# Kernel optimization log

Measured on AMD Instinct MI355X. Metric: run time of the kernel, lower is better.

Reference implementation:

```python
import jax, jax.numpy as jnp
import numpy as np

# dims: batch B, tokens T, model_dim D, expert hidden H, experts E, top-k K
B, T, D, H, E, K = 4, 2048, 2048, 2048, 8, 2
CAP_FACTOR = 1.0
S = B * T
C = int(np.ceil(K * S / E * CAP_FACTOR))  # per-expert capacity = 2048


def setup_inputs() -> dict:
    key = jax.random.key(0)
    k0, k1, k2, k3 = jax.random.split(key, 4)
    x = jax.random.normal(k0, (B, T, D), dtype=jnp.float32)
    wg = jax.random.normal(k1, (D, E), dtype=jnp.float32) * (D ** -0.5)
    w1 = jax.random.normal(k2, (E, D, H), dtype=jnp.float32) * (D ** -0.5)
    b1 = jnp.zeros((E, H), dtype=jnp.float32)
    w2 = jax.random.normal(k3, (E, H, D), dtype=jnp.float32) * (H ** -0.5)
    b2 = jnp.zeros((E, D), dtype=jnp.float32)
    return {"x": x, "wg": wg, "w1": w1, "b1": b1, "w2": w2, "b2": b2}


def _moe(x, wg, w1, b1, w2, b2):
    xt = x.reshape(S, D)
    # --- top-k gating (deepspeed-style, gates normalized over selected k) ---
    gates = jax.nn.softmax(xt @ wg, axis=-1)            # [S,E]
    vals, idx = jax.lax.top_k(gates, K)                 # [S,K]
    vals = vals / jnp.sum(vals, axis=-1, keepdims=True)
    # --- capacity-aware slot assignment (slot j offset by counts of slots < j) ---
    m = jax.nn.one_hot(idx, E, dtype=jnp.int32).transpose(1, 0, 2)  # [K,S,E]
    within = jnp.cumsum(m, axis=1) - m                  # 0-based rank within expert per slot
    counts = jnp.sum(m, axis=1)                         # [K,E]
    offs = jnp.cumsum(counts, axis=0) - counts          # [K,E] offsets from earlier slots
    loc = jnp.sum((within + offs[:, None, :]) * m, axis=2)  # [K,S]
    eid = idx.T                                         # [K,S]
    valid = loc < C
    loc_c = jnp.minimum(loc, C - 1)
    # --- dispatch: scatter raw tokens into [E,C,D] expert buffers ---
    contrib = jnp.where(valid[..., None], xt[None, :, :], 0.0)   # [K,S,D]
    disp = jnp.zeros((E, C, D), x.dtype).at[eid, loc_c].add(contrib)
    # --- grouped expert FFN: relu(x @ W1 + b1) @ W2 + b2 ---
    h = jax.nn.relu(jnp.einsum('ecd,edh->ech', disp, w1) + b1[:, None, :])
    ye = jnp.einsum('ech,ehd->ecd', h, w2) + b2[:, None, :]
    # --- combine: gather expert outputs, weight by normalized gates ---
    gathered = ye[eid, loc_c]                           # [K,S,D]
    w = (vals.T * valid).astype(x.dtype)                # [K,S]
    out = jnp.einsum('ks,ksd->sd', w, gathered)
    return out.reshape(B, T, D)


def reference(x, wg, w1, b1, w2, b2):
    y = _moe(x, wg, w1, b1, w2, b2)                     # [B,T,D]
    return jax.nn.log_softmax(jnp.sum(y, axis=2), axis=1)  # [B,T]
```

## Files before the change

### kernel.cpp

```cpp
#include <hip/hip_runtime.h>
#include <math.h>

#define S_TOK 8192
#define DDIM 2048
#define HDIM 2048
#define NE 8
#define CAP 2048
#define NBATCH 4
#define TT 2048

typedef _Float16 f16;
typedef _Float16 f16x4 __attribute__((ext_vector_type(4)));
typedef _Float16 f16x8 __attribute__((ext_vector_type(8)));
typedef float f32x4 __attribute__((ext_vector_type(4)));

typedef __attribute__((address_space(1))) const void* gas_ptr;
typedef __attribute__((address_space(3))) void* las_ptr;

__global__ __launch_bounds__(256) void gating_kernel(const float* __restrict__ x,
                                                     const float* __restrict__ wg,
                                                     int* __restrict__ eid,
                                                     float* __restrict__ wts,
                                                     int* __restrict__ slot_token,
                                                     float* __restrict__ zacc) {
  if (blockIdx.x < 64) {
    int i = blockIdx.x * 256 + threadIdx.x;
    slot_token[i] = 0;
    zacc[i] = 0.f;
  }
  int wid = threadIdx.x >> 6;
  int lane = threadIdx.x & 63;
  int s = blockIdx.x * 4 + wid;
  const float* xr = x + (size_t)s * DDIM;
  double acc[8];
#pragma unroll
  for (int e = 0; e < 8; ++e) acc[e] = 0.0;
  for (int d0 = 0; d0 < DDIM; d0 += 64) {
    float xs = xr[d0 + lane];
    const float4* wp = (const float4*)(wg + (size_t)(d0 + lane) * 8);
    float4 g0 = wp[0];
    float4 g1 = wp[1];
    double xd = (double)xs;
    acc[0] += xd * (double)g0.x; acc[1] += xd * (double)g0.y;
    acc[2] += xd * (double)g0.z; acc[3] += xd * (double)g0.w;
    acc[4] += xd * (double)g1.x; acc[5] += xd * (double)g1.y;
    acc[6] += xd * (double)g1.z; acc[7] += xd * (double)g1.w;
  }
#pragma unroll
  for (int e = 0; e < 8; ++e) {
    double v = acc[e];
    for (int off = 32; off > 0; off >>= 1) v += __shfl_down(v, off, 64);
    acc[e] = v;
  }
  if (lane == 0) {
    int e0 = 0; double l0 = acc[0];
    for (int e = 1; e < 8; ++e) if (acc[e] > l0) { l0 = acc[e]; e0 = e; }
    int e1 = -1; double l1 = -1e300;
    for (int e = 0; e < 8; ++e) if (e != e0 && acc[e] > l1) { l1 = acc[e]; e1 = e; }
    double pe = exp(l1 - l0);
    double inv = 1.0 / (1.0 + pe);
    eid[2 * s] = e0; eid[2 * s + 1] = e1;
    wts[2 * s] = (float)inv; wts[2 * s + 1] = (float)(pe * inv);
  }
}

__global__ __launch_bounds__(256) void scan_kernel(const int* __restrict__ eid,
                                                   int* __restrict__ locb,
                                                   int* __restrict__ slot_token) {
  __shared__ int seg[4][2][8];
  __shared__ int base[4][2][8];
  int tid = threadIdx.x, wid = tid >> 6, lane = tid & 63;
  unsigned long long lower = (lane == 0) ? 0ull : ((~0ull) >> (64 - lane));
  const int2* eid2 = (const int2*)eid;
  int c0 = 0, c1 = 0;
  for (int r = 0; r < 32; ++r) {
    int2 ee = eid2[wid * 2048 + r * 64 + lane];
#pragma unroll
    for (int e = 0; e < 8; ++e) {
      unsigned long long b0 = __ballot(ee.x == e);
      unsigned long long b1 = __ballot(ee.y == e);
      if (lane == e) { c0 += __popcll(b0); c1 += __popcll(b1); }
    }
  }
  if (lane < 8) { seg[wid][0][lane] = c0; seg[wid][1][lane] = c1; }
  __syncthreads();
  if (lane < 8) {
    int e = lane;
    int tot0 = seg[0][0][e] + seg[1][0][e] + seg[2][0][e] + seg[3][0][e];
    int b0 = 0, b1 = tot0;
    for (int w = 0; w < wid; ++w) { b0 += seg[w][0][e]; b1 += seg[w][1][e]; }
    base[wid][0][e] = b0; base[wid][1][e] = b1;
  }
  for (int r = 0; r < 32; ++r) {
    int2 ee = eid2[wid * 2048 + r * 64 + lane];
    int rank0 = 0, rank1 = 0, add0 = 0, add1 = 0;
#pragma unroll
    for (int e = 0; e < 8; ++e) {
      unsigned long long b0 = __ballot(ee.x == e);
      unsigned long long b1 = __ballot(ee.y == e);
      if (ee.x == e) rank0 = __popcll(b0 & lower);
      if (ee.y == e) rank1 = __popcll(b1 & lower);
      if (lane == e) { add0 = __popcll(b0); add1 = __popcll(b1); }
    }
    int loc0 = base[wid][0][ee.x] + rank0;
    int loc1 = base[wid][1][ee.y] + rank1;
    int s = wid * 2048 + r * 64 + lane;
    int2 lo; lo.x = loc0; lo.y = loc1;
    *(int2*)&locb[2 * s] = lo;
    if (loc0 < CAP) slot_token[ee.x * CAP + loc0] = s;
    if (loc1 < CAP) slot_token[ee.y * CAP + loc1] = s;
    if (lane < 8) {
      atomicAdd(&base[wid][0][lane], add0);
      atomicAdd(&base[wid][1][lane], add1);
    }
  }
}

#define W1T_BLOCKS 8192
#define W2S_BLOCKS 4096
#define ABUILD_BASE (W1T_BLOCKS + W2S_BLOCKS + 1)
__global__ __launch_bounds__(256) void prep_kernel(const float* __restrict__ w1,
                                                   const float* __restrict__ w2,
                                                   const float* __restrict__ b2,
                                                   const float* __restrict__ x,
                                                   const int* __restrict__ slot_token,
                                                   f16* __restrict__ W1T,
                                                   float* __restrict__ w2s,
                                                   float* __restrict__ b2s,
                                                   f16* __restrict__ A16) {
  __shared__ float tile[64 * 65];
  int bid = blockIdx.x, tid = threadIdx.x;
  if (bid >= ABUILD_BASE) {
    int slot = bid - ABUILD_BASE;
    int s = slot_token[slot];
    const float4* x4 = (const float4*)x + (size_t)s * 512;
    f16x4* outp = (f16x4*)(A16 + (size_t)slot * DDIM);
#pragma unroll
    for (int i = 0; i < 2; ++i) {
      int v = i * 256 + tid;
      float4 xv = x4[v];
      f16x4 h;
      h[0] = (f16)xv.x; h[1] = (f16)xv.y; h[2] = (f16)xv.z; h[3] = (f16)xv.w;
      outp[v] = h;
    }
    return;
  }
  if (bid < W1T_BLOCKS) {
    int e = bid >> 10, rem = bid & 1023;
    int d0 = (rem >> 5) << 6;
    int h0 = (rem & 31) << 6;
    const float* w1e = w1 + (size_t)e * DDIM * HDIM;
#pragma unroll
    for (int i = 0; i < 4; ++i) {
      int linear = i * 256 + tid;
      int r = linear >> 4, c4 = linear & 15;
      float4 v = *(const float4*)(w1e + (size_t)(d0 + r) * HDIM + h0 + c4 * 4);
      float* t = &tile[r * 65 + c4 * 4];
      t[0] = v.x; t[1] = v.y; t[2] = v.z; t[3] = v.w;
    }
    __syncthreads();
    f16* W1Te = W1T + (size_t)e * HDIM * DDIM;
#pragma unroll
    for (int i = 0; i < 2; ++i) {
      int linear = i * 256 + tid;
      int hr = linear >> 3, l8 = linear & 7;
      f16x8 o;
#pragma unroll
      for (int j = 0; j < 8; ++j) o[j] = (f16)tile[(l8 * 8 + j) * 65 + hr];
      *(f16x8*)(W1Te + (size_t)(h0 + hr) * DDIM + d0 + l8 * 8) = o;
    }
    return;
  }
  if (bid < W1T_BLOCKS + W2S_BLOCKS) {
    int wid = tid >> 6, lane = tid & 63;
    int row = (bid - W1T_BLOCKS) * 4 + wid;
    const float4* w24 = (const float4*)w2;
    float acc = 0.f;
    for (int j = 0; j < 8; ++j) {
      float4 v = w24[(size_t)row * 512 + j * 64 + lane];
      acc += v.x + v.y + v.z + v.w;
    }
    for (int off = 32; off > 0; off >>= 1) acc += __shfl_down(acc, off, 64);
    if (lane == 0) w2s[row] = acc;
    return;
  }
  {
    int e = tid >> 5, l32 = tid & 31;
    float acc = 0.f;
    for (int j = 0; j < 64; ++j) acc += b2[e * 2048 + j * 32 + l32];
    for (int off = 16; off > 0; off >>= 1) acc += __shfl_down(acc, off, 32);
    if (l32 == 0) b2s[e] = acc;
  }
}


template <int MB, int NB>
__device__ __forceinline__ void quad_mfma(f32x4 (&acc)[8][4], const f16x8 (&av)[4][2],
                                          const f16x8 (&bv)[2][2]) {
#pragma unroll
  for (int mf = 0; mf < 4; ++mf)
#pragma unroll
    for (int nf = 0; nf < 2; ++nf) {
      f32x4 c = acc[MB + mf][NB + nf];
      c = __builtin_amdgcn_mfma_f32_16x16x32_f16(av[mf][0], bv[nf][0], c, 0, 0, 0);
      c = __builtin_amdgcn_mfma_f32_16x16x32_f16(av[mf][1], bv[nf][1], c, 0, 0, 0);
      acc[MB + mf][NB + nf] = c;
    }
}

__device__ __forceinline__ void lda4(f16x8 (&av)[4][2], const f16* p0, const f16* p1, int mh) {
#pragma unroll
  for (int mf = 0; mf < 4; ++mf) {
    av[mf][0] = *(const f16x8*)(p0 + (mh * 4 + mf) * 1024);
    av[mf][1] = *(const f16x8*)(p1 + (mh * 4 + mf) * 1024);
  }
}
__device__ __forceinline__ void ldb2(f16x8 (&bv)[2][2], const f16* p0, const f16* p1, int nh) {
#pragma unroll
  for (int nf = 0; nf < 2; ++nf) {
    bv[nf][0] = *(const f16x8*)(p0 + (nh * 2 + nf) * 1024);
    bv[nf][1] = *(const f16x8*)(p1 + (nh * 2 + nf) * 1024);
  }
}

__device__ __forceinline__ void stage_half(const f16* tile_rows, f16* lds_region,
                                           int T, int h, int wl8, int wu8, int cs) {
#pragma unroll
  for (int i = 0; i < 2; ++i) {
    const f16* g = tile_rows + (size_t)(h * 128 + i * 64 + wl8) * DDIM + T * 64 + cs * 8;
    f16* d = lds_region + (h * 128 + i * 64 + wu8) * 64;
    __builtin_amdgcn_global_load_lds((gas_ptr)g, (las_ptr)d, 16, 0, 0);
  }
}

__device__ __forceinline__ void bar() {
  asm volatile("" ::: "memory");
  __builtin_amdgcn_s_barrier();
  asm volatile("" ::: "memory");
}
__device__ __forceinline__ void mfma_open() {
  bar();
  asm volatile("s_waitcnt lgkmcnt(0)" ::: "memory");
  __builtin_amdgcn_sched_barrier(0);
  __builtin_amdgcn_s_setprio(1);
}
__device__ __forceinline__ void mfma_close() {
  __builtin_amdgcn_s_setprio(0);
  bar();
}
__device__ __forceinline__ void mfma_close_w4() {
  __builtin_amdgcn_s_setprio(0);
  asm volatile("s_waitcnt vmcnt(4)" ::: "memory");
  bar();
}
__device__ __forceinline__ void mfma_close_w0() {
  __builtin_amdgcn_s_setprio(0);
  asm volatile("s_waitcnt vmcnt(0)" ::: "memory");
  bar();
}

__global__ __launch_bounds__(512, 2) void gemm_kernel(const f16* __restrict__ A16,
                                                      const f16* __restrict__ W1T,
                                                      const float* __restrict__ b1,
                                                      const float* __restrict__ w2s,
                                                      float* __restrict__ zacc) {
  __shared__ __align__(16) f16 lds[4 * 256 * 64];
  const int tid = threadIdx.x;
  const int wid = tid >> 6, lane = tid & 63;
  const int wm = wid >> 2, wn = wid & 3;
  const int quad = lane >> 4, l15 = lane & 15;
  const int l3 = lane >> 3, c7 = lane & 7;
  const int cs = c7 ^ l3;
  const int wl8 = wid * 8 + l3, wu8 = wid * 8;

  int bid = blockIdx.x;
  int e = bid & 7;
  int idx = bid >> 3;
  int cT = idx >> 3, hT = idx & 7;
  int c0 = cT * 256, h0 = hT * 256;

  const f16* Abase = A16 + ((size_t)e * CAP + c0) * DDIM;
  const f16* Bbase = W1T + ((size_t)e * HDIM + h0) * DDIM;

  f16* bufA0 = &lds[0];
  f16* bufB0 = &lds[16384];
  f16* bufA1 = &lds[2 * 16384];
  f16* bufB1 = &lds[3 * 16384];

  const int so0 = (quad ^ c7) * 8;
  const int so1 = ((quad + 4) ^ c7) * 8;
  const f16* a0k0 = bufA0 + (wm * 128 + l15) * 64 + so0;
  const f16* a0k1 = bufA0 + (wm * 128 + l15) * 64 + so1;
  const f16* a1k0 = a0k0 + 2 * 16384;
  const f16* a1k1 = a0k1 + 2 * 16384;
  const f16* b0k0 = bufB0 + (wn * 64 + l15) * 64 + so0;
  const f16* b0k1 = bufB0 + (wn * 64 + l15) * 64 + so1;
  const f16* b1k0 = b0k0 + 2 * 16384;
  const f16* b1k1 = b0k1 + 2 * 16384;

  f32x4 acc[8][4];
#pragma unroll
  for (int i = 0; i < 8; ++i)
#pragma unroll
    for (int jj = 0; jj < 4; ++jj) acc[i][jj] = (f32x4){0.f, 0.f, 0.f, 0.f};
  f16x8 fa[4][2], fb0[2][2], fb1[2][2];

  stage_half(Abase, bufA0, 0, 0, wl8, wu8, cs);
  stage_half(Abase, bufA0, 0, 1, wl8, wu8, cs);
  stage_half(Bbase, bufB0, 0, 0, wl8, wu8, cs);
  stage_half(Bbase, bufB0, 0, 1, wl8, wu8, cs);
  stage_half(Bbase, bufB1, 1, 0, wl8, wu8, cs);
  stage_half(Bbase, bufB1, 1, 1, wl8, wu8, cs);
  asm volatile("s_waitcnt vmcnt(4)" ::: "memory");
  bar();

#pragma unroll 1
  for (int it = 0; it < 15; ++it) {
    const int Ta = 2 * it + 1, Tb = 2 * it + 2, Tc = 2 * it + 3;
    lda4(fa, a0k0, a0k1, 0);
    ldb2(fb0, b0k0, b0k1, 0);
    stage_half(Abase, bufA1, Ta, 0, wl8, wu8, cs);
    mfma_open(); quad_mfma<0, 0>(acc, fa, fb0); mfma_close();

    ldb2(fb1, b0k0, b0k1, 1);
    stage_half(Abase, bufA1, Ta, 1, wl8, wu8, cs);
    mfma_open(); quad_mfma<0, 2>(acc, fa, fb1); mfma_close();

    lda4(fa, a0k0, a0k1, 1);
    stage_half(Bbase, bufB0, Tb, 0, wl8, wu8, cs);
    mfma_open(); quad_mfma<4, 2>(acc, fa, fb1); mfma_close();

    stage_half(Bbase, bufB0, Tb, 1, wl8, wu8, cs);
    mfma_open(); quad_mfma<4, 0>(acc, fa, fb0); mfma_close_w4();

    lda4(fa, a1k0, a1k1, 0);
    ldb2(fb0, b1k0, b1k1, 0);
    stage_half(Abase, bufA0, Tb, 0, wl8, wu8, cs);
    mfma_open(); quad_mfma<0, 0>(acc, fa, fb0); mfma_close();

    ldb2(fb1, b1k0, b1k1, 1);
    stage_half(Abase, bufA0, Tb, 1, wl8, wu8, cs);
    mfma_open(); quad_mfma<0, 2>(acc, fa, fb1); mfma_close();

    lda4(fa, a1k0, a1k1, 1);
    stage_half(Bbase, bufB1, Tc, 0, wl8, wu8, cs);
    mfma_open(); quad_mfma<4, 2>(acc, fa, fb1); mfma_close();

    stage_half(Bbase, bufB1, Tc, 1, wl8, wu8, cs);
    mfma_open(); quad_mfma<4, 0>(acc, fa, fb0); mfma_close_w4();
  }
  {
    lda4(fa, a0k0, a0k1, 0);
    ldb2(fb0, b0k0, b0k1, 0);
    stage_half(Abase, bufA1, 31, 0, wl8, wu8, cs);
    mfma_open(); quad_mfma<0, 0>(acc, fa, fb0); mfma_close();

    ldb2(fb1, b0k0, b0k1, 1);
    stage_half(Abase, bufA1, 31, 1, wl8, wu8, cs);
    mfma_open(); quad_mfma<0, 2>(acc, fa, fb1); mfma_close();

    lda4(fa, a0k0, a0k1, 1);
    mfma_open(); quad_mfma<4, 2>(acc, fa, fb1); mfma_close();

    mfma_open(); quad_mfma<4, 0>(acc, fa, fb0); mfma_close_w0();

    lda4(fa, a1k0, a1k1, 0);
    ldb2(fb0, b1k0, b1k1, 0);
    mfma_open(); quad_mfma<0, 0>(acc, fa, fb0); mfma_close();

    ldb2(fb1, b1k0, b1k1, 1);
    mfma_open(); quad_mfma<0, 2>(acc, fa, fb1); mfma_close();

    lda4(fa, a1k0, a1k1, 1);
    mfma_open(); quad_mfma<4, 2>(acc, fa, fb1); mfma_close();

    mfma_open(); quad_mfma<4, 0>(acc, fa, fb0);
    __builtin_amdgcn_s_setprio(0);
  }

  float b1v[4], wsv[4];
#pragma unroll
  for (int nf = 0; nf < 4; ++nf) {
    int h = h0 + wn * 64 + nf * 16 + l15;
    b1v[nf] = b1[e * HDIM + h];
    wsv[nf] = w2s[e * HDIM + h];
  }
#pragma unroll
  for (int mf = 0; mf < 8; ++mf) {
    float pr[4];
#pragma unroll
    for (int rr = 0; rr < 4; ++rr) {
      float t = 0.f;
#pragma unroll
      for (int nf = 0; nf < 4; ++nf) {
        float v = acc[mf][nf][rr] + b1v[nf];
        t += (v > 0.f ? v : 0.f) * wsv[nf];
      }
      pr[rr] = t;
    }
#pragma unroll
    for (int rr = 0; rr < 4; ++rr)
#pragma unroll
      for (int off = 1; off < 16; off <<= 1) pr[rr] += __shfl_xor(pr[rr], off, 64);
    if (l15 == 0) {
      int m = c0 + wm * 128 + mf * 16 + quad * 4;
#pragma unroll
      for (int rr = 0; rr < 4; ++rr) atomicAdd(&zacc[e * CAP + m + rr], pr[rr]);
    }
  }
}

__global__ __launch_bounds__(256) void tail_kernel(const int* __restrict__ eid,
                                                   const int* __restrict__ locb,
                                                   const float* __restrict__ wts,
                                                   const float* __restrict__ zacc,
                                                   const float* __restrict__ b2s,
                                                   float* __restrict__ out) {
  __shared__ float red[4];
  int b = blockIdx.x, tid = threadIdx.x;
  int wid = tid >> 6, lane = tid & 63;
  float v[8];
  float mx = -1e30f;
#pragma unroll
  for (int i = 0; i < 8; ++i) {
    int s = b * TT + i * 256 + tid;
    float zz = 0.f;
#pragma unroll
    for (int k = 0; k < 2; ++k) {
      int e = eid[2 * s + k], loc = locb[2 * s + k];
      if (loc < CAP) zz += wts[2 * s + k] * (zacc[e * CAP + loc] + b2s[e]);
    }
    v[i] = zz;
    mx = fmaxf(mx, zz);
  }
  for (int off = 32; off > 0; off >>= 1) mx = fmaxf(mx, __shfl_xor(mx, off, 64));
  if (lane == 0) red[wid] = mx;
  __syncthreads();
  mx = fmaxf(fmaxf(red[0], red[1]), fmaxf(red[2], red[3]));
  float sum = 0.f;
#pragma unroll
  for (int i = 0; i < 8; ++i) sum += expf(v[i] - mx);
  for (int off = 32; off > 0; off >>= 1) sum += __shfl_xor(sum, off, 64);
  __syncthreads();
  if (lane == 0) red[wid] = sum;
  __syncthreads();
  sum = red[0] + red[1] + red[2] + red[3];
  float lse = mx + logf(sum);
#pragma unroll
  for (int i = 0; i < 8; ++i) out[b * TT + i * 256 + tid] = v[i] - lse;
}

extern "C" void kernel_launch(void* const* d_in, const int* in_sizes, int n_in,
                              void* d_out, int out_size, void* d_ws, size_t ws_size,
                              hipStream_t stream) {
  const float* x  = (const float*)d_in[0];
  const float* wg = (const float*)d_in[1];
  const float* w1 = (const float*)d_in[2];
  const float* b1 = (const float*)d_in[3];
  const float* w2 = (const float*)d_in[4];
  const float* b2 = (const float*)d_in[5];
  float* out = (float*)d_out;

  char* ws = (char*)d_ws;
  size_t off = 0;
  auto alloc = [&](size_t bytes) -> char* {
    char* p = ws + off;
    off += (bytes + 255) & ~(size_t)255;
    return p;
  };
  f16* A16 = (f16*)alloc((size_t)NE * CAP * DDIM * 2);
  f16* W1T = (f16*)alloc((size_t)NE * HDIM * DDIM * 2);
  float* w2s = (float*)alloc((size_t)NE * HDIM * 4);
  float* b2s = (float*)alloc(NE * 4);
  int* eid = (int*)alloc((size_t)S_TOK * 2 * 4);
  float* wts = (float*)alloc((size_t)S_TOK * 2 * 4);
  int* locb = (int*)alloc((size_t)S_TOK * 2 * 4);
  int* slot_token = (int*)alloc((size_t)NE * CAP * 4);
  float* zacc = (float*)alloc((size_t)NE * CAP * 4);
  if (off > ws_size) return;

  gating_kernel<<<S_TOK / 4, 256, 0, stream>>>(x, wg, eid, wts, slot_token, zacc);
  scan_kernel<<<1, 256, 0, stream>>>(eid, locb, slot_token);
  prep_kernel<<<ABUILD_BASE + NE * CAP, 256, 0, stream>>>(w1, w2, b2, x, slot_token,
                                                          W1T, w2s, b2s, A16);
  gemm_kernel<<<NE * 64, 512, 0, stream>>>(A16, W1T, b1, w2s, zacc);
  tail_kernel<<<NBATCH, 256, 0, stream>>>(eid, locb, wts, zacc, b2s, out);
}
```

Baseline: 545.8 us.

## Fuse gating into weight-prep kernel and split A-buffer build into own kernel

Gating now runs inside the weight-preparation launch as extra blocks, so the W1 transpose/convert and w2/b2 reductions overlap with gating instead of waiting behind it. The gather of tokens into the fp16 expert buffer moves to a separate kernel that runs after the scan and uses one wave per slot. The tail kernel goes from 256 to 1024 threads per block to spread its work wider. This changes the launch order and dependencies (the scan now waits on the larger fused kernel) and adds one more kernel launch.

After: 541.4 us. Within noise of the previous version (-0.8%).

```diff
diff --git a/kernel.cpp b/kernel.cpp
--- a/kernel.cpp
+++ b/kernel.cpp
@@ -17,50 +17,113 @@
 typedef __attribute__((address_space(1))) const void* gas_ptr;
 typedef __attribute__((address_space(3))) void* las_ptr;
 
-__global__ __launch_bounds__(256) void gating_kernel(const float* __restrict__ x,
-                                                     const float* __restrict__ wg,
-                                                     int* __restrict__ eid,
-                                                     float* __restrict__ wts,
-                                                     int* __restrict__ slot_token,
-                                                     float* __restrict__ zacc) {
-  if (blockIdx.x < 64) {
-    int i = blockIdx.x * 256 + threadIdx.x;
-    slot_token[i] = 0;
-    zacc[i] = 0.f;
-  }
-  int wid = threadIdx.x >> 6;
-  int lane = threadIdx.x & 63;
-  int s = blockIdx.x * 4 + wid;
-  const float* xr = x + (size_t)s * DDIM;
-  double acc[8];
-#pragma unroll
-  for (int e = 0; e < 8; ++e) acc[e] = 0.0;
-  for (int d0 = 0; d0 < DDIM; d0 += 64) {
-    float xs = xr[d0 + lane];
-    const float4* wp = (const float4*)(wg + (size_t)(d0 + lane) * 8);
-    float4 g0 = wp[0];
-    float4 g1 = wp[1];
-    double xd = (double)xs;
-    acc[0] += xd * (double)g0.x; acc[1] += xd * (double)g0.y;
-    acc[2] += xd * (double)g0.z; acc[3] += xd * (double)g0.w;
-    acc[4] += xd * (double)g1.x; acc[5] += xd * (double)g1.y;
-    acc[6] += xd * (double)g1.z; acc[7] += xd * (double)g1.w;
-  }
-#pragma unroll
-  for (int e = 0; e < 8; ++e) {
-    double v = acc[e];
-    for (int off = 32; off > 0; off >>= 1) v += __shfl_down(v, off, 64);
-    acc[e] = v;
-  }
-  if (lane == 0) {
-    int e0 = 0; double l0 = acc[0];
-    for (int e = 1; e < 8; ++e) if (acc[e] > l0) { l0 = acc[e]; e0 = e; }
-    int e1 = -1; double l1 = -1e300;
-    for (int e = 0; e < 8; ++e) if (e != e0 && acc[e] > l1) { l1 = acc[e]; e1 = e; }
-    double pe = exp(l1 - l0);
-    double inv = 1.0 / (1.0 + pe);
-    eid[2 * s] = e0; eid[2 * s + 1] = e1;
-    wts[2 * s] = (float)inv; wts[2 * s + 1] = (float)(pe * inv);
+#define W1T_BLOCKS 8192
+#define W2S_BLOCKS 4096
+#define GATE_BASE (W1T_BLOCKS + W2S_BLOCKS + 1)
+#define K1_GRID (GATE_BASE + S_TOK / 4)
+
+__global__ __launch_bounds__(256) void prep_kernel(const float* __restrict__ w1,
+                                                   const float* __restrict__ w2,
+                                                   const float* __restrict__ b2,
+                                                   const float* __restrict__ x,
+                                                   const float* __restrict__ wg,
+                                                   int* __restrict__ eid,
+                                                   float* __restrict__ wts,
+                                                   int* __restrict__ slot_token,
+                                                   float* __restrict__ zacc,
+                                                   f16* __restrict__ W1T,
+                                                   float* __restrict__ w2s,
+                                                   float* __restrict__ b2s) {
+  __shared__ float tile[64 * 65];
+  int bid = blockIdx.x, tid = threadIdx.x;
+  if (bid >= GATE_BASE) {
+    int g = bid - GATE_BASE;
+    if (g < 64) {
+      int i = g * 256 + tid;
+      slot_token[i] = 0;
+      zacc[i] = 0.f;
+    }
+    int wid = tid >> 6;
+    int lane = tid & 63;
+    int s = g * 4 + wid;
+    const float* xr = x + (size_t)s * DDIM;
+    double acc[8];
+#pragma unroll
+    for (int e = 0; e < 8; ++e) acc[e] = 0.0;
+    for (int d0 = 0; d0 < DDIM; d0 += 64) {
+      float xs = xr[d0 + lane];
+      const float4* wp = (const float4*)(wg + (size_t)(d0 + lane) * 8);
+      float4 g0 = wp[0];
+      float4 g1 = wp[1];
+      double xd = (double)xs;
+      acc[0] += xd * (double)g0.x; acc[1] += xd * (double)g0.y;
+      acc[2] += xd * (double)g0.z; acc[3] += xd * (double)g0.w;
+      acc[4] += xd * (double)g1.x; acc[5] += xd * (double)g1.y;
+      acc[6] += xd * (double)g1.z; acc[7] += xd * (double)g1.w;
+    }
+#pragma unroll
+    for (int e = 0; e < 8; ++e) {
+      double v = acc[e];
+      for (int off = 32; off > 0; off >>= 1) v += __shfl_down(v, off, 64);
+      acc[e] = v;
+    }
+    if (lane == 0) {
+      int e0 = 0; double l0 = acc[0];
+      for (int e = 1; e < 8; ++e) if (acc[e] > l0) { l0 = acc[e]; e0 = e; }
+      int e1 = -1; double l1 = -1e300;
+      for (int e = 0; e < 8; ++e) if (e != e0 && acc[e] > l1) { l1 = acc[e]; e1 = e; }
+      double pe = exp(l1 - l0);
+      double inv = 1.0 / (1.0 + pe);
+      eid[2 * s] = e0; eid[2 * s + 1] = e1;
+      wts[2 * s] = (float)inv; wts[2 * s + 1] = (float)(pe * inv);
+    }
+    return;
+  }
+  if (bid < W1T_BLOCKS) {
+    int e = bid >> 10, rem = bid & 1023;
+    int d0 = (rem >> 5) << 6;
+    int h0 = (rem & 31) << 6;
+    const float* w1e = w1 + (size_t)e * DDIM * HDIM;
+#pragma unroll
+    for (int i = 0; i < 4; ++i) {
+      int linear = i * 256 + tid;
+      int r = linear >> 4, c4 = linear & 15;
+      float4 v = *(const float4*)(w1e + (size_t)(d0 + r) * HDIM + h0 + c4 * 4);
+      float* t = &tile[r * 65 + c4 * 4];
+      t[0] = v.x; t[1] = v.y; t[2] = v.z; t[3] = v.w;
+    }
+    __syncthreads();
+    f16* W1Te = W1T + (size_t)e * HDIM * DDIM;
+#pragma unroll
+    for (int i = 0; i < 2; ++i) {
+      int linear = i * 256 + tid;
+      int hr = linear >> 3, l8 = linear & 7;
+      f16x8 o;
+#pragma unroll
+      for (int j = 0; j < 8; ++j) o[j] = (f16)tile[(l8 * 8 + j) * 65 + hr];
+      *(f16x8*)(W1Te + (size_t)(h0 + hr) * DDIM + d0 + l8 * 8) = o;
+    }
+    return;
+  }
+  if (bid < W1T_BLOCKS + W2S_BLOCKS) {
+    int wid = tid >> 6, lane = tid & 63;
+    int row = (bid - W1T_BLOCKS) * 4 + wid;
+    const float4* w24 = (const float4*)w2;
+    float acc = 0.f;
+    for (int j = 0; j < 8; ++j) {
+      float4 v = w24[(size_t)row * 512 + j * 64 + lane];
+      acc += v.x + v.y + v.z + v.w;
+    }
+    for (int off = 32; off > 0; off >>= 1) acc += __shfl_down(acc, off, 64);
+    if (lane == 0) w2s[row] = acc;
+    return;
+  }
+  {
+    int e = tid >> 5, l32 = tid & 31;
+    float acc = 0.f;
+    for (int j = 0; j < 64; ++j) acc += b2[e * 2048 + j * 32 + l32];
+    for (int off = 16; off > 0; off >>= 1) acc += __shfl_down(acc, off, 32);
+    if (l32 == 0) b2s[e] = acc;
   }
 }
 
@@ -116,80 +179,20 @@
   }
 }
 
-#define W1T_BLOCKS 8192
-#define W2S_BLOCKS 4096
-#define ABUILD_BASE (W1T_BLOCKS + W2S_BLOCKS + 1)
-__global__ __launch_bounds__(256) void prep_kernel(const float* __restrict__ w1,
-                                                   const float* __restrict__ w2,
-                                                   const float* __restrict__ b2,
-                                                   const float* __restrict__ x,
-                                                   const int* __restrict__ slot_token,
-                                                   f16* __restrict__ W1T,
-                                                   float* __restrict__ w2s,
-                                                   float* __restrict__ b2s,
-                                                   f16* __restrict__ A16) {
-  __shared__ float tile[64 * 65];
-  int bid = blockIdx.x, tid = threadIdx.x;
-  if (bid >= ABUILD_BASE) {
-    int slot = bid - ABUILD_BASE;
-    int s = slot_token[slot];
-    const float4* x4 = (const float4*)x + (size_t)s * 512;
-    f16x4* outp = (f16x4*)(A16 + (size_t)slot * DDIM);
-#pragma unroll
-    for (int i = 0; i < 2; ++i) {
-      int v = i * 256 + tid;
-      float4 xv = x4[v];
-      f16x4 h;
-      h[0] = (f16)xv.x; h[1] = (f16)xv.y; h[2] = (f16)xv.z; h[3] = (f16)xv.w;
-      outp[v] = h;
-    }
-    return;
-  }
-  if (bid < W1T_BLOCKS) {
-    int e = bid >> 10, rem = bid & 1023;
-    int d0 = (rem >> 5) << 6;
-    int h0 = (rem & 31) << 6;
-    const float* w1e = w1 + (size_t)e * DDIM * HDIM;
-#pragma unroll
-    for (int i = 0; i < 4; ++i) {
-      int linear = i * 256 + tid;
-      int r = linear >> 4, c4 = linear & 15;
-      float4 v = *(const float4*)(w1e + (size_t)(d0 + r) * HDIM + h0 + c4 * 4);
-      float* t = &tile[r * 65 + c4 * 4];
-      t[0] = v.x; t[1] = v.y; t[2] = v.z; t[3] = v.w;
-    }
-    __syncthreads();
-    f16* W1Te = W1T + (size_t)e * HDIM * DDIM;
-#pragma unroll
-    for (int i = 0; i < 2; ++i) {
-      int linear = i * 256 + tid;
-      int hr = linear >> 3, l8 = linear & 7;
-      f16x8 o;
-#pragma unroll
-      for (int j = 0; j < 8; ++j) o[j] = (f16)tile[(l8 * 8 + j) * 65 + hr];
-      *(f16x8*)(W1Te + (size_t)(h0 + hr) * DDIM + d0 + l8 * 8) = o;
-    }
-    return;
-  }
-  if (bid < W1T_BLOCKS + W2S_BLOCKS) {
-    int wid = tid >> 6, lane = tid & 63;
-    int row = (bid - W1T_BLOCKS) * 4 + wid;
-    const float4* w24 = (const float4*)w2;
-    float acc = 0.f;
-    for (int j = 0; j < 8; ++j) {
-      float4 v = w24[(size_t)row * 512 + j * 64 + lane];
-      acc += v.x + v.y + v.z + v.w;
-    }
-    for (int off = 32; off > 0; off >>= 1) acc += __shfl_down(acc, off, 64);
-    if (lane == 0) w2s[row] = acc;
-    return;
-  }
-  {
-    int e = tid >> 5, l32 = tid & 31;
-    float acc = 0.f;
-    for (int j = 0; j < 64; ++j) acc += b2[e * 2048 + j * 32 + l32];
-    for (int off = 16; off > 0; off >>= 1) acc += __shfl_down(acc, off, 32);
-    if (l32 == 0) b2s[e] = acc;
+__global__ __launch_bounds__(256) void abuild_kernel(const float* __restrict__ x,
+                                                     const int* __restrict__ slot_token,
+                                                     f16* __restrict__ A16) {
+  int wid = threadIdx.x >> 6, lane = threadIdx.x & 63;
+  int slot = blockIdx.x * 4 + wid;
+  int s = slot_token[slot];
+  const float4* x4 = (const float4*)x + (size_t)s * 512 + lane;
+  f16x4* outp = (f16x4*)(A16 + (size_t)slot * DDIM) + lane;
+#pragma unroll
+  for (int i = 0; i < 8; ++i) {
+    float4 xv = x4[i * 64];
+    f16x4 h;
+    h[0] = (f16)xv.x; h[1] = (f16)xv.y; h[2] = (f16)xv.z; h[3] = (f16)xv.w;
+    outp[i * 64] = h;
   }
 }
 
@@ -410,20 +413,20 @@
   }
 }
 
-__global__ __launch_bounds__(256) void tail_kernel(const int* __restrict__ eid,
-                                                   const int* __restrict__ locb,
-                                                   const float* __restrict__ wts,
-                                                   const float* __restrict__ zacc,
-                                                   const float* __restrict__ b2s,
-                                                   float* __restrict__ out) {
-  __shared__ float red[4];
+__global__ __launch_bounds__(1024) void tail_kernel(const int* __restrict__ eid,
+                                                    const int* __restrict__ locb,
+                                                    const float* __restrict__ wts,
+                                                    const float* __restrict__ zacc,
+                                                    const float* __restrict__ b2s,
+                                                    float* __restrict__ out) {
+  __shared__ float red[16];
   int b = blockIdx.x, tid = threadIdx.x;
   int wid = tid >> 6, lane = tid & 63;
-  float v[8];
+  float v[2];
   float mx = -1e30f;
 #pragma unroll
-  for (int i = 0; i < 8; ++i) {
-    int s = b * TT + i * 256 + tid;
+  for (int i = 0; i < 2; ++i) {
+    int s = b * TT + i * 1024 + tid;
     float zz = 0.f;
 #pragma unroll
     for (int k = 0; k < 2; ++k) {
@@ -436,18 +439,20 @@
   for (int off = 32; off > 0; off >>= 1) mx = fmaxf(mx, __shfl_xor(mx, off, 64));
   if (lane == 0) red[wid] = mx;
   __syncthreads();
-  mx = fmaxf(fmaxf(red[0], red[1]), fmaxf(red[2], red[3]));
-  float sum = 0.f;
-#pragma unroll
-  for (int i = 0; i < 8; ++i) sum += expf(v[i] - mx);
+  mx = red[0];
+#pragma unroll
+  for (int j = 1; j < 16; ++j) mx = fmaxf(mx, red[j]);
+  float sum = expf(v[0] - mx) + expf(v[1] - mx);
   for (int off = 32; off > 0; off >>= 1) sum += __shfl_xor(sum, off, 64);
   __syncthreads();
   if (lane == 0) red[wid] = sum;
   __syncthreads();
-  sum = red[0] + red[1] + red[2] + red[3];
+  sum = 0.f;
+#pragma unroll
+  for (int j = 0; j < 16; ++j) sum += red[j];
   float lse = mx + logf(sum);
 #pragma unroll
-  for (int i = 0; i < 8; ++i) out[b * TT + i * 256 + tid] = v[i] - lse;
+  for (int i = 0; i < 2; ++i) out[b * TT + i * 1024 + tid] = v[i] - lse;
 }
 
 extern "C" void kernel_launch(void* const* d_in, const int* in_sizes, int n_in,
@@ -479,10 +484,10 @@
   float* zacc = (float*)alloc((size_t)NE * CAP * 4);
   if (off > ws_size) return;
 
-  gating_kernel<<<S_TOK / 4, 256, 0, stream>>>(x, wg, eid, wts, slot_token, zacc);
+  prep_kernel<<<K1_GRID, 256, 0, stream>>>(w1, w2, b2, x, wg, eid, wts, slot_token, zacc,
+                                           W1T, w2s, b2s);
   scan_kernel<<<1, 256, 0, stream>>>(eid, locb, slot_token);
-  prep_kernel<<<ABUILD_BASE + NE * CAP, 256, 0, stream>>>(w1, w2, b2, x, slot_token,
-                                                          W1T, w2s, b2s, A16);
+  abuild_kernel<<<NE * CAP / 4, 256, 0, stream>>>(x, slot_token, A16);
   gemm_kernel<<<NE * 64, 512, 0, stream>>>(A16, W1T, b1, w2s, zacc);
-  tail_kernel<<<NBATCH, 256, 0, stream>>>(eid, locb, wts, zacc, b2s, out);
-}
+  tail_kernel<<<NBATCH, 1024, 0, stream>>>(eid, locb, wts, zacc, b2s, out);
+}
```
